# Kernel optimization log

Measured on AMD Instinct MI355X. Metric: run time of the kernel, lower is better.

## Reference

```python
import jax, jax.numpy as jnp
import numpy as np
import math

HID = 128      # hidden_dim == d_inner (expand=1)
NSTATE = 8     # d_state
K = 4          # scan directions
RANK = math.ceil(HID / 16)  # dt_rank = 8
B, H, W = 4, 64, 64


def _ln(x, g, b, eps=1e-5):
    m = jnp.mean(x, -1, keepdims=True)
    v = jnp.mean((x - m) ** 2, -1, keepdims=True)
    return (x - m) * jax.lax.rsqrt(v + eps) * g + b


def _ss2d(x, in_w, conv_w, conv_b, xproj_w, dt_w, dt_b, A_logs, Ds, ln_g, ln_b, out_w):
    # x: [B,H,W,C] -> VMamba SS2D with d_inner=C, 4-direction selective scan
    Bn, Hh, Ww, C = x.shape
    D, L = C, Hh * Ww
    N = A_logs.shape[-1]
    R = dt_w.shape[-1]
    xz = x @ in_w.T                      # [B,H,W,2D]
    xc, z = jnp.split(xz, 2, axis=-1)
    xc = xc.transpose(0, 3, 1, 2)        # [B,D,H,W]
    xc = jax.lax.conv_general_dilated(xc, conv_w, (1, 1), 'SAME', feature_group_count=D)
    xc = jax.nn.silu(xc + conv_b[None, :, None, None])
    x_hw = xc.reshape(Bn, D, L)
    x_wh = xc.transpose(0, 1, 3, 2).reshape(Bn, D, L)
    xs = jnp.stack([x_hw, x_wh, x_hw[..., ::-1], x_wh[..., ::-1]], 1)  # [B,K,D,L]
    x_dbl = jnp.einsum('bkdl,kcd->bkcl', xs, xproj_w)
    dts, Bs, Cs = x_dbl[:, :, :R], x_dbl[:, :, R:R + N], x_dbl[:, :, R + N:]
    dt = jax.nn.softplus(jnp.einsum('bkrl,kdr->bkdl', dts, dt_w) + dt_b[None, :, :, None])
    A = -jnp.exp(A_logs.reshape(K, D, N))  # [K,D,N]

    def step(h, inp):
        x_t, dt_t, B_t, C_t = inp          # [B,K,D],[B,K,D],[B,K,N],[B,K,N]
        h = h * jnp.exp(dt_t[..., None] * A) + dt_t[..., None] * B_t[:, :, None, :] * x_t[..., None]
        return h, jnp.einsum('bkdn,bkn->bkd', h, C_t)

    h0 = jnp.zeros((Bn, K, D, N), x.dtype)
    _, ys = jax.lax.scan(step, h0, (xs.transpose(3, 0, 1, 2), dt.transpose(3, 0, 1, 2),
                                    Bs.transpose(3, 0, 1, 2), Cs.transpose(3, 0, 1, 2)))
    out_y = ys.transpose(1, 2, 3, 0) + Ds.reshape(K, D)[None, :, :, None] * xs  # [B,K,D,L]
    wh_y = out_y[:, 3, :, ::-1].reshape(Bn, D, Ww, Hh).transpose(0, 1, 3, 2).reshape(Bn, D, L)
    invwh_y = out_y[:, 1].reshape(Bn, D, Ww, Hh).transpose(0, 1, 3, 2).reshape(Bn, D, L)
    y = out_y[:, 0] + out_y[:, 2, :, ::-1] + wh_y + invwh_y
    y = _ln(y.transpose(0, 2, 1).reshape(Bn, Hh, Ww, D), ln_g, ln_b)
    return (y * jax.nn.silu(z)) @ out_w.T


def _enhance(x, g, b, w, bias):
    return jax.nn.gelu(_ln(x, g, b) @ w.T + bias, approximate=False)


def setup_inputs() -> dict:
    key = jax.random.key(0)
    ks = jax.random.split(key, 12)
    f = lambda k, s, sc=0.02: jax.random.normal(k, s, jnp.float32) * sc
    return dict(
        sar_feat=jax.random.normal(ks[0], (B, H, W, HID), jnp.float32),
        opt_feat=jax.random.normal(ks[1], (B, H, W, HID), jnp.float32),
        ss_in_w=f(ks[2], (2, 2 * HID, HID)),
        ss_conv_w=f(ks[3], (2, HID, 1, 3, 3), 0.1),
        ss_conv_b=f(ks[4], (2, HID)),
        ss_xproj_w=f(ks[5], (2, K, RANK + 2 * NSTATE, HID)),
        ss_dt_w=f(ks[6], (2, K, HID, RANK), 0.1),
        ss_dt_b=f(ks[7], (2, K, HID), 0.1),
        ss_Alogs=jnp.tile(jnp.log(jnp.arange(1, NSTATE + 1, dtype=jnp.float32)), (2, K * HID, 1)),
        ss_Ds=jnp.ones((2, K * HID), jnp.float32),
        ss_ln_g=jnp.ones((2, HID), jnp.float32),
        ss_ln_b=jnp.zeros((2, HID), jnp.float32),
        ss_out_w=f(ks[8], (2, HID, HID)),
        enh_ln_g=jnp.ones((2, HID), jnp.float32),
        enh_ln_b=jnp.zeros((2, HID), jnp.float32),
        enh_w=f(ks[9], (2, HID, HID)),
        enh_b=jnp.zeros((2, HID), jnp.float32),
    )


def reference(sar_feat, opt_feat, ss_in_w, ss_conv_w, ss_conv_b, ss_xproj_w, ss_dt_w,
              ss_dt_b, ss_Alogs, ss_Ds, ss_ln_g, ss_ln_b, ss_out_w,
              enh_ln_g, enh_ln_b, enh_w, enh_b):
    # cat([opt,sar],-1)[...,:C] == opt ; cat([sar,opt],-1)[...,:C] == sar (faithful identity slice)
    # index 0 = cross_ss2d_s2o (input opt), index 1 = cross_ss2d_o2s (input sar)
    xin = jnp.stack([opt_feat, sar_feat])
    guided = jax.vmap(_ss2d)(xin, ss_in_w, ss_conv_w, ss_conv_b, ss_xproj_w, ss_dt_w,
                             ss_dt_b, ss_Alogs, ss_Ds, ss_ln_g, ss_ln_b, ss_out_w)
    # enhance params: index 0 = enhance_sar (on sar_guided=guided[1]), index 1 = enhance_opt (on opt_guided=guided[0])
    enh_in = jnp.stack([guided[1], guided[0]])
    enhanced = jax.vmap(_enhance)(enh_in, enh_ln_g, enh_ln_b, enh_w, enh_b)
    return (sar_feat + enhanced[0], opt_feat + enhanced[1])
```

## Files before the change

### kernel.cpp

```cpp
#include <hip/hip_runtime.h>
#include <hip/hip_bf16.h>
#include <math.h>

#define DEV __device__ __forceinline__

static constexpr int LL = 4096;
static constexpr int DD = 128;
static constexpr int SEG = 128;
static constexpr float LOG2E = 1.4426950408889634f;
static constexpr float LN2 = 0.6931471805599453f;

DEV float silu_(float x) { return x / (1.f + __expf(-x)); }
DEV float erf_(float x) {
  const float ax = fabsf(x);
  const float t = 1.f / fmaf(0.3275911f, ax, 1.f);
  float p = fmaf(1.061405429f, t, -1.453152027f);
  p = fmaf(p, t, 1.421413741f);
  p = fmaf(p, t, -0.284496736f);
  p = fmaf(p, t, 0.254829592f);
  p = p * t;
  const float r = 1.f - p * __expf(-ax * ax);
  return x < 0.f ? -r : r;
}
DEV float gelu_(float x) { return 0.5f * x * (1.f + erf_(x * 0.7071067811865475f)); }
DEV float sp_(float x) {
  const float t = __builtin_amdgcn_exp2f(-fabsf(x) * LOG2E);
  return fmaxf(x, 0.f) + LN2 * __builtin_amdgcn_logf(1.f + t);
}

template <int CTRL>
DEV float dpp_add_(float x) {
  int y = __builtin_amdgcn_update_dpp(0, __float_as_int(x), CTRL, 0xF, 0xF, true);
  return x + __int_as_float(y);
}

DEV void seg_base_step(int k, int s, int& base, int& step) {
  if (k == 0)      { base = s * 64;        step = 1;   }
  else if (k == 1) { base = s;             step = 64;  }
  else if (k == 2) { base = 4095 - s * 64; step = -1;  }
  else             { base = 4095 - s;      step = -64; }
}

__global__ __launch_bounds__(256) void k_inproj(
    const float* __restrict__ sar, const float* __restrict__ opt,
    const float* __restrict__ in_w, float* __restrict__ xz) {
  const int lt = blockIdx.x, ct = blockIdx.y, mb = blockIdx.z;
  const int m = mb >> 2;
  const float* __restrict__ x = (m == 0 ? opt : sar) + (size_t)(mb & 3) * (LL * DD);
  const float* __restrict__ W = in_w + (size_t)m * 256 * DD;
  __shared__ float sA[64][68];
  __shared__ float sW[64][68];
  const int tid = threadIdx.x;
  const int tc = tid & 15, tl = tid >> 4;
  float acc[4][4] = {};
  for (int db = 0; db < 2; ++db) {
    __syncthreads();
    for (int idx = tid; idx < 64 * 16; idx += 256) {
      const int r = idx >> 4, d4 = (idx & 15) << 2;
      *(float4*)&sA[r][d4] = *(const float4*)&x[(size_t)(lt * 64 + r) * DD + db * 64 + d4];
      *(float4*)&sW[r][d4] = *(const float4*)&W[(size_t)(ct * 64 + r) * DD + db * 64 + d4];
    }
    __syncthreads();
#pragma unroll 4
    for (int d = 0; d < 64; d += 4) {
      float4 a[4], w[4];
#pragma unroll
      for (int q = 0; q < 4; ++q) a[q] = *(const float4*)&sA[tl * 4 + q][d];
#pragma unroll
      for (int j = 0; j < 4; ++j) w[j] = *(const float4*)&sW[tc + 16 * j][d];
#pragma unroll
      for (int j = 0; j < 4; ++j)
#pragma unroll
        for (int q = 0; q < 4; ++q)
          acc[j][q] += a[q].x * w[j].x + a[q].y * w[j].y + a[q].z * w[j].z + a[q].w * w[j].w;
    }
  }
  float* __restrict__ dst = xz + ((size_t)mb * 256 + ct * 64) * LL + lt * 64;
#pragma unroll
  for (int j = 0; j < 4; ++j) {
    float4 v = make_float4(acc[j][0], acc[j][1], acc[j][2], acc[j][3]);
    *(float4*)&dst[(size_t)(tc + 16 * j) * LL + tl * 4] = v;
  }
}

__global__ __launch_bounds__(256) void k_conv(
    const float* __restrict__ xz, const float* __restrict__ conv_w,
    const float* __restrict__ conv_b, float* __restrict__ xc) {
  const int ht = blockIdx.x, dg = blockIdx.y, mb = blockIdx.z;
  const int m = mb >> 2;
  __shared__ float sIn[8][18][66];
  __shared__ float sOut[1024][8];
  const float* __restrict__ src = xz + ((size_t)mb * 256 + dg * 8) * LL;
  const int tid = threadIdx.x;
  for (int idx = tid; idx < 8 * 18 * 66; idx += 256) {
    const int dd = idx / (18 * 66);
    const int rem = idx - dd * (18 * 66);
    const int hh = rem / 66, ww = rem - hh * 66;
    const int h = ht * 16 + hh - 1, w = ww - 1;
    float v = 0.f;
    if (h >= 0 && h < 64 && w >= 0 && w < 64) v = src[(size_t)dd * LL + h * 64 + w];
    sIn[dd][hh][ww] = v;
  }
  __syncthreads();
  const int dd = tid & 7, wv = tid >> 3;
  const int dch = dg * 8 + dd;
  float wk[9];
#pragma unroll
  for (int t = 0; t < 9; ++t) wk[t] = conv_w[((size_t)m * DD + dch) * 9 + t];
  const float bias = conv_b[m * DD + dch];
  for (int hh = 0; hh < 16; ++hh) {
#pragma unroll
    for (int wh = 0; wh < 2; ++wh) {
      const int w = wv + wh * 32;
      float s = bias;
#pragma unroll
      for (int kh = 0; kh < 3; ++kh)
#pragma unroll
        for (int kw = 0; kw < 3; ++kw)
          s = fmaf(sIn[dd][hh + kh][w + kw], wk[kh * 3 + kw], s);
      sOut[hh * 64 + w][dd] = silu_(s);
    }
  }
  __syncthreads();
  float* __restrict__ dst = xc + (size_t)mb * LL * DD + dg * 8;
#pragma unroll
  for (int r = 0; r < 4; ++r) {
    const int pos = tid + r * 256;
    const int l = ht * 1024 + pos;
    *(float4*)&dst[(size_t)l * DD + 0] = *(const float4*)&sOut[pos][0];
    *(float4*)&dst[(size_t)l * DD + 4] = *(const float4*)&sOut[pos][4];
  }
}

__global__ __launch_bounds__(256) void k_xproj(
    const float* __restrict__ xc, const float* __restrict__ xproj_w,
    float* __restrict__ xdbl) {
  const int lt = blockIdx.x, k = blockIdx.y, mb = blockIdx.z;
  const int m = mb >> 2, mbk = mb * 4 + k;
  __shared__ float sX[64][132];
  __shared__ float sW[24][132];
  const int tid = threadIdx.x;
  const float* __restrict__ src = xc + (size_t)mb * LL * DD;
  int base, step;
  seg_base_step(k, lt, base, step);
  for (int idx = tid; idx < 64 * 32; idx += 256) {
    const int l = idx >> 5, d4 = (idx & 31) << 2;
    *(float4*)&sX[l][d4] = *(const float4*)&src[(size_t)(base + l * step) * DD + d4];
  }
  const float* __restrict__ Wsrc = xproj_w + ((size_t)m * 4 + k) * 24 * DD;
  for (int idx = tid; idx < 24 * 32; idx += 256) {
    const int r = idx >> 5, d4 = (idx & 31) << 2;
    *(float4*)&sW[r][d4] = *(const float4*)&Wsrc[(size_t)r * DD + d4];
  }
  __syncthreads();
  const int l = tid >> 2, cg = tid & 3;
  float acc[6] = {};
#pragma unroll 8
  for (int d = 0; d < 128; d += 4) {
    const float4 xv = *(const float4*)&sX[l][d];
#pragma unroll
    for (int j = 0; j < 6; ++j) {
      const float4 wv = *(const float4*)&sW[cg * 6 + j][d];
      acc[j] += xv.x * wv.x + xv.y * wv.y + xv.z * wv.z + xv.w * wv.w;
    }
  }
  float* __restrict__ dst = xdbl + ((size_t)mbk * LL + lt * 64 + l) * 24 + cg * 6;
#pragma unroll
  for (int j = 0; j < 6; ++j) dst[j] = acc[j];
}

DEV void load_aln2(const float* __restrict__ Alogs, int m, int k, int d,
                   float* __restrict__ aln2, bool& fastp) {
  const float4 a0 = *(const float4*)&Alogs[((size_t)m * 512 + k * DD + d) * 8];
  const float4 a1 = *(const float4*)&Alogs[((size_t)m * 512 + k * DD + d) * 8 + 4];
  aln2[0] = -__expf(a0.x) * LOG2E; aln2[1] = -__expf(a0.y) * LOG2E;
  aln2[2] = -__expf(a0.z) * LOG2E; aln2[3] = -__expf(a0.w) * LOG2E;
  aln2[4] = -__expf(a1.x) * LOG2E; aln2[5] = -__expf(a1.y) * LOG2E;
  aln2[6] = -__expf(a1.z) * LOG2E; aln2[7] = -__expf(a1.w) * LOG2E;
  fastp = true;
#pragma unroll
  for (int n = 1; n < 8; ++n)
    fastp = fastp && (fabsf(aln2[n] - (float)(n + 1) * aln2[0]) <=
                      1e-4f * fabsf(aln2[n]) + 1e-12f);
}

DEV void load_w8(const float* __restrict__ dt_w, int mbk, int d,
                 float* __restrict__ wreg) {
  const float4 w0 = *(const float4*)&dt_w[((size_t)mbk * DD + d) * 8];
  const float4 w1 = *(const float4*)&dt_w[((size_t)mbk * DD + d) * 8 + 4];
  wreg[0] = w0.x; wreg[1] = w0.y; wreg[2] = w0.z; wreg[3] = w0.w;
  wreg[4] = w1.x; wreg[5] = w1.y; wreg[6] = w1.z; wreg[7] = w1.w;
}

template <bool FAST>
DEV void qpow_(float dt, const float* __restrict__ aln2, float* __restrict__ q) {
  if constexpr (FAST) {
    q[0] = __builtin_amdgcn_exp2f(dt * aln2[0]);
    q[1] = q[0] * q[0]; q[2] = q[1] * q[0]; q[3] = q[1] * q[1];
    q[4] = q[3] * q[0]; q[5] = q[3] * q[1]; q[6] = q[3] * q[2]; q[7] = q[3] * q[3];
  } else {
#pragma unroll
    for (int n = 0; n < 8; ++n) q[n] = __builtin_amdgcn_exp2f(dt * aln2[n]);
  }
}

DEV float dt_of_(const float* __restrict__ t24,
                 const float* __restrict__ w, float bw) {
  const float4 t0 = *(const float4*)&t24[0];
  const float4 t1 = *(const float4*)&t24[4];
  float s = bw;
  s = fmaf(t0.x, w[0], s); s = fmaf(t0.y, w[1], s);
  s = fmaf(t0.z, w[2], s); s = fmaf(t0.w, w[3], s);
  s = fmaf(t1.x, w[4], s); s = fmaf(t1.y, w[5], s);
  s = fmaf(t1.z, w[6], s); s = fmaf(t1.w, w[7], s);
  return sp_(s);
}

template <bool FAST>
DEV void hstep_(const float* __restrict__ t24, float dt, float x,
                const float* __restrict__ aln2, float* __restrict__ h) {
  const float u = dt * x;
  float q[8];
  qpow_<FAST>(dt, aln2, q);
  const float4 b0 = *(const float4*)&t24[8];
  const float4 b1 = *(const float4*)&t24[12];
  h[0] = fmaf(h[0], q[0], u * b0.x);
  h[1] = fmaf(h[1], q[1], u * b0.y);
  h[2] = fmaf(h[2], q[2], u * b0.z);
  h[3] = fmaf(h[3], q[3], u * b0.w);
  h[4] = fmaf(h[4], q[4], u * b1.x);
  h[5] = fmaf(h[5], q[5], u * b1.y);
  h[6] = fmaf(h[6], q[6], u * b1.z);
  h[7] = fmaf(h[7], q[7], u * b1.w);
}

template <bool FAST>
DEV float ystep_(const float* __restrict__ t24, float dt, float x,
                 const float* __restrict__ aln2, float dsv,
                 float* __restrict__ h) {
  const float u = dt * x;
  float q[8];
  qpow_<FAST>(dt, aln2, q);
  const float4 b0 = *(const float4*)&t24[8];
  const float4 b1 = *(const float4*)&t24[12];
  const float4 c0 = *(const float4*)&t24[16];
  const float4 c1 = *(const float4*)&t24[20];
  float y = dsv * x;
  h[0] = fmaf(h[0], q[0], u * b0.x); y = fmaf(h[0], c0.x, y);
  h[1] = fmaf(h[1], q[1], u * b0.y); y = fmaf(h[1], c0.y, y);
  h[2] = fmaf(h[2], q[2], u * b0.z); y = fmaf(h[2], c0.z, y);
  h[3] = fmaf(h[3], q[3], u * b0.w); y = fmaf(h[3], c0.w, y);
  h[4] = fmaf(h[4], q[4], u * b1.x); y = fmaf(h[4], c1.x, y);
  h[5] = fmaf(h[5], q[5], u * b1.y); y = fmaf(h[5], c1.y, y);
  h[6] = fmaf(h[6], q[6], u * b1.z); y = fmaf(h[6], c1.z, y);
  h[7] = fmaf(h[7], q[7], u * b1.w); y = fmaf(h[7], c1.w, y);
  return y;
}

template <bool FAST>
DEV void loop1d_(const float* __restrict__ tA, const float* __restrict__ tB,
                 const float* __restrict__ sx, int d,
                 const float* __restrict__ aln2A, const float* __restrict__ aln2B,
                 const float* __restrict__ wA, const float* __restrict__ wB,
                 float bwA, float bwB, float* __restrict__ hA,
                 float* __restrict__ hB, float& dtsA, float& dtsB) {
#pragma unroll 8
  for (int j = 0; j < 32; ++j) {
    const float xA = sx[j * 128 + d];
    const float xB = sx[(31 - j) * 128 + d];
    const float dtA = dt_of_(tA + j * 24, wA, bwA);
    const float dtB = dt_of_(tB + j * 24, wB, bwB);
    dtsA += dtA; dtsB += dtB;
    hstep_<FAST>(tA + j * 24, dtA, xA, aln2A, hA);
    hstep_<FAST>(tB + j * 24, dtB, xB, aln2B, hB);
  }
}

__global__ __launch_bounds__(128) void k_scan1(
    const float* __restrict__ xc, const float* __restrict__ xdbl,
    const float* __restrict__ dt_w, const float* __restrict__ dt_b,
    const float* __restrict__ Alogs, float* __restrict__ hend,
    float* __restrict__ Pseg) {
  const int s = blockIdx.x, p = blockIdx.y, mb = blockIdx.z;
  const int m = mb >> 2;
  const int kA = p, kB = p + 2;
  const int sA = s, sB = 127 - s;
  const int mbkA = mb * 4 + kA, mbkB = mb * 4 + kB;
  const int d = threadIdx.x;
  __shared__ float sx[32 * 128];

  const float* __restrict__ tA = xdbl + ((size_t)mbkA * LL + sA * 32) * 24;
  const float* __restrict__ tB = xdbl + ((size_t)mbkB * LL + sB * 32) * 24;

  const int base0 = (p == 0) ? s * 32 : ((s & 1) * 32) * 64 + (s >> 1);
  const int stepPos = (p == 0) ? 1 : 64;
  const float* __restrict__ xsrc = xc + (size_t)mb * LL * DD;
#pragma unroll
  for (int t = 0; t < 8; ++t) {
    const int idx = d + t * 128;
    const int r = idx >> 5, c4 = (idx & 31) << 2;
    ((float4*)sx)[idx] = *(const float4*)&xsrc[(size_t)(base0 + r * stepPos) * DD + c4];
  }

  float aln2A[8], aln2B[8]; bool fA, fB;
  load_aln2(Alogs, m, kA, d, aln2A, fA);
  load_aln2(Alogs, m, kB, d, aln2B, fB);
  float wA[8], wB[8];
  load_w8(dt_w, mbkA, d, wA);
  load_w8(dt_w, mbkB, d, wB);
  const float bwA = dt_b[(size_t)mbkA * DD + d];
  const float bwB = dt_b[(size_t)mbkB * DD + d];
  __syncthreads();

  float hA[8] = {0, 0, 0, 0, 0, 0, 0, 0};
  float hB[8] = {0, 0, 0, 0, 0, 0, 0, 0};
  float dtsA = 0.f, dtsB = 0.f;
  if (fA && fB)
    loop1d_<true>(tA, tB, sx, d, aln2A, aln2B, wA, wB, bwA, bwB, hA, hB, dtsA, dtsB);
  else
    loop1d_<false>(tA, tB, sx, d, aln2A, aln2B, wA, wB, bwA, bwB, hA, hB, dtsA, dtsB);

  {
    float* __restrict__ he = hend + (((size_t)mbkA * SEG + sA) << 10) + d * 8;
    float* __restrict__ pe = Pseg + (((size_t)mbkA * SEG + sA) << 10) + d * 8;
    *(float4*)&he[0] = make_float4(hA[0], hA[1], hA[2], hA[3]);
    *(float4*)&he[4] = make_float4(hA[4], hA[5], hA[6], hA[7]);
    *(float4*)&pe[0] = make_float4(
        __builtin_amdgcn_exp2f(aln2A[0] * dtsA), __builtin_amdgcn_exp2f(aln2A[1] * dtsA),
        __builtin_amdgcn_exp2f(aln2A[2] * dtsA), __builtin_amdgcn_exp2f(aln2A[3] * dtsA));
    *(float4*)&pe[4] = make_float4(
        __builtin_amdgcn_exp2f(aln2A[4] * dtsA), __builtin_amdgcn_exp2f(aln2A[5] * dtsA),
        __builtin_amdgcn_exp2f(aln2A[6] * dtsA), __builtin_amdgcn_exp2f(aln2A[7] * dtsA));
  }
  {
    float* __restrict__ he = hend + (((size_t)mbkB * SEG + sB) << 10) + d * 8;
    float* __restrict__ pe = Pseg + (((size_t)mbkB * SEG + sB) << 10) + d * 8;
    *(float4*)&he[0] = make_float4(hB[0], hB[1], hB[2], hB[3]);
    *(float4*)&he[4] = make_float4(hB[4], hB[5], hB[6], hB[7]);
    *(float4*)&pe[0] = make_float4(
        __builtin_amdgcn_exp2f(aln2B[0] * dtsB), __builtin_amdgcn_exp2f(aln2B[1] * dtsB),
        __builtin_amdgcn_exp2f(aln2B[2] * dtsB), __builtin_amdgcn_exp2f(aln2B[3] * dtsB));
    *(float4*)&pe[4] = make_float4(
        __builtin_amdgcn_exp2f(aln2B[4] * dtsB), __builtin_amdgcn_exp2f(aln2B[5] * dtsB),
        __builtin_amdgcn_exp2f(aln2B[6] * dtsB), __builtin_amdgcn_exp2f(aln2B[7] * dtsB));
  }
}

__global__ __launch_bounds__(256) void k_scan2(
    const float* __restrict__ hend, const float* __restrict__ Pseg,
    float* __restrict__ hin) {
  const int gid = blockIdx.x * 256 + threadIdx.x;
  const int mbk = gid >> 10, dn = gid & 1023;
  const float* __restrict__ P = Pseg + ((size_t)mbk * SEG << 10) + dn;
  const float* __restrict__ E = hend + ((size_t)mbk * SEG << 10) + dn;
  float* __restrict__ O = hin + ((size_t)mbk * SEG << 10) + dn;
  float h = 0.f;
  for (int c0 = 0; c0 < SEG; c0 += 16) {
    float pv[16], ev[16];
#pragma unroll
    for (int t = 0; t < 16; ++t) {
      pv[t] = P[(size_t)(c0 + t) << 10];
      ev[t] = E[(size_t)(c0 + t) << 10];
    }
#pragma unroll
    for (int t = 0; t < 16; ++t) {
      O[(size_t)(c0 + t) << 10] = h;
      h = fmaf(pv[t], h, ev[t]);
    }
  }
}

template <bool FAST>
DEV void chainA_(const float* __restrict__ t24, const float* __restrict__ sx, int d,
                 const float* __restrict__ aln2, const float* __restrict__ w,
                 float bw, float dsv, float* __restrict__ h,
                 float* __restrict__ va) {
#pragma unroll
  for (int j = 0; j < 32; ++j) {
    const float x = sx[j * 128 + d];
    const float dt = dt_of_(t24 + j * 24, w, bw);
    va[j] = ystep_<FAST>(t24 + j * 24, dt, x, aln2, dsv, h);
  }
}

template <bool FAST>
DEV void chainB_(const float* __restrict__ t24, const float* __restrict__ sx, int d,
                 const float* __restrict__ aln2, const float* __restrict__ w,
                 float bw, float dsv, float* __restrict__ h,
                 const float* __restrict__ va, float* __restrict__ yd,
                 ptrdiff_t sstep) {
#pragma unroll
  for (int j = 0; j < 32; ++j) {
    const int phys = 31 - j;
    const float x = sx[phys * 128 + d];
    const float dt = dt_of_(t24 + j * 24, w, bw);
    const float v = ystep_<FAST>(t24 + j * 24, dt, x, aln2, dsv, h);
    yd[(ptrdiff_t)phys * sstep] = v + va[phys];
  }
}

__global__ __launch_bounds__(128) void k_scan3(
    const float* __restrict__ xc, const float* __restrict__ xdbl,
    const float* __restrict__ dt_w, const float* __restrict__ dt_b,
    const float* __restrict__ Alogs, const float* __restrict__ Ds,
    const float* __restrict__ hin, float* __restrict__ yrow,
    float* __restrict__ ycol) {
  const int s = blockIdx.x, p = blockIdx.y, mb = blockIdx.z;
  const int m = mb >> 2;
  const int kA = p, kB = p + 2;
  const int sA = s, sB = 127 - s;
  const int mbkA = mb * 4 + kA, mbkB = mb * 4 + kB;
  const int d = threadIdx.x;
  __shared__ float sx[32 * 128];

  const float* __restrict__ tA = xdbl + ((size_t)mbkA * LL + sA * 32) * 24;
  const float* __restrict__ tB = xdbl + ((size_t)mbkB * LL + sB * 32) * 24;

  const int base0 = (p == 0) ? s * 32 : ((s & 1) * 32) * 64 + (s >> 1);
  const int stepPos = (p == 0) ? 1 : 64;
  const float* __restrict__ xsrc = xc + (size_t)mb * LL * DD;
#pragma unroll
  for (int t = 0; t < 8; ++t) {
    const int idx = d + t * 128;
    const int r = idx >> 5, c4 = (idx & 31) << 2;
    ((float4*)sx)[idx] = *(const float4*)&xsrc[(size_t)(base0 + r * stepPos) * DD + c4];
  }

  float aln2A[8], aln2B[8]; bool fA, fB;
  load_aln2(Alogs, m, kA, d, aln2A, fA);
  load_aln2(Alogs, m, kB, d, aln2B, fB);
  float wA[8], wB[8];
  load_w8(dt_w, mbkA, d, wA);
  load_w8(dt_w, mbkB, d, wB);
  const float bwA = dt_b[(size_t)mbkA * DD + d];
  const float bwB = dt_b[(size_t)mbkB * DD + d];
  const float dsvA = Ds[(size_t)m * 512 + kA * DD + d];
  const float dsvB = Ds[(size_t)m * 512 + kB * DD + d];

  float hA[8], hB[8];
  {
    const float* hp = hin + (((size_t)mbkA * SEG + sA) << 10) + d * 8;
    const float4 h0 = *(const float4*)&hp[0];
    const float4 h1 = *(const float4*)&hp[4];
    hA[0] = h0.x; hA[1] = h0.y; hA[2] = h0.z; hA[3] = h0.w;
    hA[4] = h1.x; hA[5] = h1.y; hA[6] = h1.z; hA[7] = h1.w;
  }
  {
    const float* hp = hin + (((size_t)mbkB * SEG + sB) << 10) + d * 8;
    const float4 h0 = *(const float4*)&hp[0];
    const float4 h1 = *(const float4*)&hp[4];
    hB[0] = h0.x; hB[1] = h0.y; hB[2] = h0.z; hB[3] = h0.w;
    hB[4] = h1.x; hB[5] = h1.y; hB[6] = h1.z; hB[7] = h1.w;
  }

  const size_t off0 = (size_t)mb * LL * DD + (size_t)base0 * DD + d;
  float* __restrict__ yd = (p == 0 ? yrow : ycol) + off0;
  const ptrdiff_t sstep = (ptrdiff_t)stepPos * DD;
  __syncthreads();

  float va[32];
  if (fA) chainA_<true>(tA, sx, d, aln2A, wA, bwA, dsvA, hA, va);
  else    chainA_<false>(tA, sx, d, aln2A, wA, bwA, dsvA, hA, va);
  if (fB) chainB_<true>(tB, sx, d, aln2B, wB, bwB, dsvB, hB, va, yd, sstep);
  else    chainB_<false>(tB, sx, d, aln2B, wB, bwB, dsvB, hB, va, yd, sstep);
}

__global__ __launch_bounds__(256) void k_outproj(
    const float* __restrict__ yrow, const float* __restrict__ ycol,
    const float* __restrict__ xz, const float* __restrict__ ln_g,
    const float* __restrict__ ln_b, const float* __restrict__ out_w,
    float* __restrict__ guided) {
  const int lt = blockIdx.x, mb = blockIdx.y;
  const int m = mb >> 2;
  __shared__ float sv[32][132];
  __shared__ float sW[64][68];
  __shared__ float smr[32][2];
  __shared__ float sg[128], sb[128];
  const int tid = threadIdx.x;
  const size_t yoff = ((size_t)mb * LL + lt * 32) * DD;
  const float4* p0 = (const float4*)(yrow + yoff);
  const float4* p1 = (const float4*)(ycol + yoff);
  float4 ya[4], yb[4];
#pragma unroll
  for (int t = 0; t < 4; ++t) { ya[t] = p0[tid + t * 256]; yb[t] = p1[tid + t * 256]; }
  const int zc = tid >> 1, zh = tid & 1;
  const float4* zsrc = (const float4*)(xz + ((size_t)mb * 256 + 128 + zc) * LL + lt * 32 + zh * 16);
  float4 zv[4];
#pragma unroll
  for (int t = 0; t < 4; ++t) zv[t] = zsrc[t];
  const float* __restrict__ Wp = out_w + (size_t)m * DD * DD;
  float4 wpre[4];
#pragma unroll
  for (int t = 0; t < 4; ++t) {
    const int idx = tid + t * 256;
    wpre[t] = *(const float4*)&Wp[(size_t)(idx >> 4) * DD + ((idx & 15) << 2)];
  }
  if (tid < 128) { sg[tid] = ln_g[m * DD + tid]; sb[tid] = ln_b[m * DD + tid]; }
#pragma unroll
  for (int t = 0; t < 4; ++t) {
    const int idx = tid + t * 256;
    float4 v;
    v.x = ya[t].x + yb[t].x; v.y = ya[t].y + yb[t].y;
    v.z = ya[t].z + yb[t].z; v.w = ya[t].w + yb[t].w;
    *(float4*)&sv[idx >> 5][(idx & 31) << 2] = v;
  }
  __syncthreads();
  {
    const int l = tid >> 3, q = tid & 7;
    float s = 0.f, s2 = 0.f;
#pragma unroll
    for (int d0 = 0; d0 < 16; d0 += 4) {
      const float4 v = *(const float4*)&sv[l][q * 16 + d0];
      s += v.x + v.y + v.z + v.w;
      s2 += v.x * v.x + v.y * v.y + v.z * v.z + v.w * v.w;
    }
    s = dpp_add_<0xB1>(s); s = dpp_add_<0x4E>(s); s = dpp_add_<0x141>(s);
    s2 = dpp_add_<0xB1>(s2); s2 = dpp_add_<0x4E>(s2); s2 = dpp_add_<0x141>(s2);
    if (q == 0) {
      const float mean = s * (1.f / 128.f);
      smr[l][0] = mean;
      smr[l][1] = rsqrtf(fmaf(s2, 1.f / 128.f, -mean * mean) + 1e-5f);
    }
  }
  __syncthreads();
  {
    const float g = sg[zc], bb = sb[zc];
    const float* zf = (const float*)zv;
#pragma unroll
    for (int i2 = 0; i2 < 16; ++i2) {
      const int l = zh * 16 + i2;
      const float v = fmaf((sv[l][zc] - smr[l][0]) * smr[l][1], g, bb);
      sv[l][zc] = v * silu_(zf[i2]);
    }
  }
  const int tc = tid & 15, tl = tid >> 4;
  float* __restrict__ dst = guided + ((size_t)mb * LL + lt * 32) * DD;
  float accA[4][2] = {}, accB[4][2] = {};
#pragma unroll
  for (int jb = 0; jb < 2; ++jb) {
#pragma unroll
    for (int db = 0; db < 2; ++db) {
      __syncthreads();
#pragma unroll
      for (int t = 0; t < 4; ++t) {
        const int idx = tid + t * 256;
        *(float4*)&sW[idx >> 4][(idx & 15) << 2] = wpre[t];
      }
      const int ph = jb * 2 + db + 1;
      if (ph < 4) {
        const int jb2 = ph >> 1, db2 = ph & 1;
#pragma unroll
        for (int t = 0; t < 4; ++t) {
          const int idx = tid + t * 256;
          wpre[t] = *(const float4*)&Wp[(size_t)(jb2 * 64 + (idx >> 4)) * DD + db2 * 64 + ((idx & 15) << 2)];
        }
      }
      __syncthreads();
      float (*acc)[2] = (jb == 0) ? accA : accB;
#pragma unroll 4
      for (int d0 = 0; d0 < 64; d0 += 4) {
        float4 av[2], wv[4];
#pragma unroll
        for (int q = 0; q < 2; ++q) av[q] = *(const float4*)&sv[tl * 2 + q][db * 64 + d0];
#pragma unroll
        for (int j = 0; j < 4; ++j) wv[j] = *(const float4*)&sW[tc + 16 * j][d0];
#pragma unroll
        for (int j = 0; j < 4; ++j)
#pragma unroll
          for (int q = 0; q < 2; ++q)
            acc[j][q] += av[q].x * wv[j].x + av[q].y * wv[j].y + av[q].z * wv[j].z + av[q].w * wv[j].w;
      }
    }
  }
  __syncthreads();
#pragma unroll
  for (int jb = 0; jb < 2; ++jb)
#pragma unroll
    for (int j = 0; j < 4; ++j)
#pragma unroll
      for (int q = 0; q < 2; ++q)
        sv[tl * 2 + q][jb * 64 + tc + 16 * j] = (jb == 0) ? accA[j][q] : accB[j][q];
  __syncthreads();
#pragma unroll
  for (int t = 0; t < 4; ++t) {
    const int idx = tid + t * 256;
    const int row = idx >> 5, c4 = (idx & 31) << 2;
    *(float4*)&dst[(size_t)row * DD + c4] = *(const float4*)&sv[row][c4];
  }
}

__global__ __launch_bounds__(256) void k_enhance(
    const float* __restrict__ guided, const float* __restrict__ eg,
    const float* __restrict__ ebv, const float* __restrict__ ew,
    const float* __restrict__ ebias, const float* __restrict__ sar,
    const float* __restrict__ opt, float* __restrict__ outp) {
  const int lt = blockIdx.x, ib = blockIdx.y;
  const int i = ib >> 2, b = ib & 3;
  __shared__ float sv[32][132];
  __shared__ float sW[64][68];
  __shared__ float smr[32][2];
  __shared__ float sg[128], sb2[128], sbias[128];
  const int tid = threadIdx.x;
  const float4* gsrc =
      (const float4*)(guided + (((size_t)(1 - i) * 4 + b) * LL + lt * 32) * DD);
  float4 gv[4];
#pragma unroll
  for (int t = 0; t < 4; ++t) gv[t] = gsrc[tid + t * 256];
  const float* __restrict__ resid = (i == 0 ? sar : opt) + ((size_t)b * LL + lt * 32) * DD;
  float4 rv4[4];
#pragma unroll
  for (int t = 0; t < 4; ++t) {
    const int idx = tid + t * 256;
    rv4[t] = *(const float4*)&resid[(size_t)(idx >> 5) * DD + ((idx & 31) << 2)];
  }
  const float* __restrict__ Wp = ew + (size_t)i * DD * DD;
  float4 wpre[4];
#pragma unroll
  for (int t = 0; t < 4; ++t) {
    const int idx = tid + t * 256;
    wpre[t] = *(const float4*)&Wp[(size_t)(idx >> 4) * DD + ((idx & 15) << 2)];
  }
  if (tid < 128) {
    sg[tid] = eg[i * DD + tid];
    sb2[tid] = ebv[i * DD + tid];
    sbias[tid] = ebias[i * DD + tid];
  }
#pragma unroll
  for (int t = 0; t < 4; ++t) {
    const int idx = tid + t * 256;
    *(float4*)&sv[idx >> 5][(idx & 31) << 2] = gv[t];
  }
  __syncthreads();
  {
    const int l = tid >> 3, q = tid & 7;
    float s = 0.f, s2 = 0.f;
#pragma unroll
    for (int d0 = 0; d0 < 16; d0 += 4) {
      const float4 v = *(const float4*)&sv[l][q * 16 + d0];
      s += v.x + v.y + v.z + v.w;
      s2 += v.x * v.x + v.y * v.y + v.z * v.z + v.w * v.w;
    }
    s = dpp_add_<0xB1>(s); s = dpp_add_<0x4E>(s); s = dpp_add_<0x141>(s);
    s2 = dpp_add_<0xB1>(s2); s2 = dpp_add_<0x4E>(s2); s2 = dpp_add_<0x141>(s2);
    if (q == 0) {
      const float mean = s * (1.f / 128.f);
      smr[l][0] = mean;
      smr[l][1] = rsqrtf(fmaf(s2, 1.f / 128.f, -mean * mean) + 1e-5f);
    }
  }
  __syncthreads();
  {
    const int c = tid >> 1, half = tid & 1;
    const float g = sg[c], bb = sb2[c];
#pragma unroll
    for (int i2 = 0; i2 < 16; ++i2) {
      const int l = half * 16 + i2;
      sv[l][c] = fmaf((sv[l][c] - smr[l][0]) * smr[l][1], g, bb);
    }
  }
  const int tc = tid & 15, tl = tid >> 4;
  float* __restrict__ dst = outp + (size_t)i * (4 * LL * DD) + ((size_t)b * LL + lt * 32) * DD;
  float accA[4][2] = {}, accB[4][2] = {};
#pragma unroll
  for (int jb = 0; jb < 2; ++jb) {
#pragma unroll
    for (int db = 0; db < 2; ++db) {
      __syncthreads();
#pragma unroll
      for (int t = 0; t < 4; ++t) {
        const int idx = tid + t * 256;
        *(float4*)&sW[idx >> 4][(idx & 15) << 2] = wpre[t];
      }
      const int ph = jb * 2 + db + 1;
      if (ph < 4) {
        const int jb2 = ph >> 1, db2 = ph & 1;
#pragma unroll
        for (int t = 0; t < 4; ++t) {
          const int idx = tid + t * 256;
          wpre[t] = *(const float4*)&Wp[(size_t)(jb2 * 64 + (idx >> 4)) * DD + db2 * 64 + ((idx & 15) << 2)];
        }
      }
      __syncthreads();
      float (*acc)[2] = (jb == 0) ? accA : accB;
#pragma unroll 4
      for (int d0 = 0; d0 < 64; d0 += 4) {
        float4 av[2], wv[4];
#pragma unroll
        for (int q = 0; q < 2; ++q) av[q] = *(const float4*)&sv[tl * 2 + q][db * 64 + d0];
#pragma unroll
        for (int j = 0; j < 4; ++j) wv[j] = *(const float4*)&sW[tc + 16 * j][d0];
#pragma unroll
        for (int j = 0; j < 4; ++j)
#pragma unroll
          for (int q = 0; q < 2; ++q)
            acc[j][q] += av[q].x * wv[j].x + av[q].y * wv[j].y + av[q].z * wv[j].z + av[q].w * wv[j].w;
      }
    }
  }
  __syncthreads();
#pragma unroll
  for (int jb = 0; jb < 2; ++jb)
#pragma unroll
    for (int j = 0; j < 4; ++j)
#pragma unroll
      for (int q = 0; q < 2; ++q)
        sv[tl * 2 + q][jb * 64 + tc + 16 * j] = (jb == 0) ? accA[j][q] : accB[j][q];
  __syncthreads();
#pragma unroll
  for (int t = 0; t < 4; ++t) {
    const int idx = tid + t * 256;
    const int row = idx >> 5, c4 = (idx & 31) << 2;
    const float4 a = *(const float4*)&sv[row][c4];
    const float4 bia = *(const float4*)&sbias[c4];
    float4 o;
    o.x = rv4[t].x + gelu_(a.x + bia.x);
    o.y = rv4[t].y + gelu_(a.y + bia.y);
    o.z = rv4[t].z + gelu_(a.z + bia.z);
    o.w = rv4[t].w + gelu_(a.w + bia.w);
    *(float4*)&dst[(size_t)row * DD + c4] = o;
  }
}

extern "C" void kernel_launch(void* const* d_in, const int* in_sizes, int n_in,
                              void* d_out, int out_size, void* d_ws, size_t ws_size,
                              hipStream_t stream) {
  (void)in_sizes; (void)n_in; (void)out_size; (void)ws_size;
  const float* sar    = (const float*)d_in[0];
  const float* opt    = (const float*)d_in[1];
  const float* in_w   = (const float*)d_in[2];
  const float* conv_w = (const float*)d_in[3];
  const float* conv_b = (const float*)d_in[4];
  const float* xproj_w= (const float*)d_in[5];
  const float* dt_w   = (const float*)d_in[6];
  const float* dt_b   = (const float*)d_in[7];
  const float* Alogs  = (const float*)d_in[8];
  const float* Ds     = (const float*)d_in[9];
  const float* ln_g   = (const float*)d_in[10];
  const float* ln_b   = (const float*)d_in[11];
  const float* out_w  = (const float*)d_in[12];
  const float* eg     = (const float*)d_in[13];
  const float* eb     = (const float*)d_in[14];
  const float* ew     = (const float*)d_in[15];
  const float* ebias  = (const float*)d_in[16];

  float* ws     = (float*)d_ws;
  float* xz     = ws;
  float* xc     = xz + 8388608;
  float* xdbl   = xc + 4194304;
  float* yrowb  = xdbl + 3145728;
  float* ycolb  = yrowb + 4194304;
  float* guided = ycolb + 4194304;
  float* hend   = guided + 4194304;
  float* Pseg   = hend + 4194304;
  float* hin    = Pseg + 4194304;
  float* outf   = (float*)d_out;

  k_inproj <<<dim3(64, 4, 8), 256, 0, stream>>>(sar, opt, in_w, xz);
  k_conv   <<<dim3(4, 16, 8), 256, 0, stream>>>(xz, conv_w, conv_b, xc);
  k_xproj  <<<dim3(64, 4, 8), 256, 0, stream>>>(xc, xproj_w, xdbl);
  k_scan1  <<<dim3(128, 2, 8), 128, 0, stream>>>(xc, xdbl, dt_w, dt_b, Alogs, hend, Pseg);
  k_scan2  <<<dim3(128), 256, 0, stream>>>(hend, Pseg, hin);
  k_scan3  <<<dim3(128, 2, 8), 128, 0, stream>>>(xc, xdbl, dt_w, dt_b, Alogs, Ds, hin,
                                                 yrowb, ycolb);
  k_outproj<<<dim3(128, 8), 256, 0, stream>>>(yrowb, ycolb, xz, ln_g, ln_b, out_w, guided);
  k_enhance<<<dim3(128, 8), 256, 0, stream>>>(guided, eg, eb, ew, ebias, sar, opt, outf);
}
```

Measured before the change: 266.0 us.

## Precompute dt in fp16 once and fuse paired-direction xproj

```diff
diff --git a/kernel.cpp b/kernel.cpp
--- a/kernel.cpp
+++ b/kernel.cpp
@@ -1,5 +1,6 @@
 #include <hip/hip_runtime.h>
 #include <hip/hip_bf16.h>
+#include <hip/hip_fp16.h>
 #include <math.h>
 
 #define DEV __device__ __forceinline__
@@ -135,38 +136,46 @@
 __global__ __launch_bounds__(256) void k_xproj(
     const float* __restrict__ xc, const float* __restrict__ xproj_w,
     float* __restrict__ xdbl) {
-  const int lt = blockIdx.x, k = blockIdx.y, mb = blockIdx.z;
-  const int m = mb >> 2, mbk = mb * 4 + k;
+  const int lt = blockIdx.x, p = blockIdx.y, mb = blockIdx.z;
+  const int m = mb >> 2;
+  const int mbkA = mb * 4 + p, mbkB = mb * 4 + p + 2;
   __shared__ float sX[64][132];
-  __shared__ float sW[24][132];
+  __shared__ float sWA[24][132];
+  __shared__ float sWB[24][132];
   const int tid = threadIdx.x;
   const float* __restrict__ src = xc + (size_t)mb * LL * DD;
   int base, step;
-  seg_base_step(k, lt, base, step);
+  seg_base_step(p, lt, base, step);
   for (int idx = tid; idx < 64 * 32; idx += 256) {
     const int l = idx >> 5, d4 = (idx & 31) << 2;
     *(float4*)&sX[l][d4] = *(const float4*)&src[(size_t)(base + l * step) * DD + d4];
   }
-  const float* __restrict__ Wsrc = xproj_w + ((size_t)m * 4 + k) * 24 * DD;
+  const float* __restrict__ WsA = xproj_w + ((size_t)m * 4 + p) * 24 * DD;
+  const float* __restrict__ WsB = xproj_w + ((size_t)m * 4 + p + 2) * 24 * DD;
   for (int idx = tid; idx < 24 * 32; idx += 256) {
     const int r = idx >> 5, d4 = (idx & 31) << 2;
-    *(float4*)&sW[r][d4] = *(const float4*)&Wsrc[(size_t)r * DD + d4];
+    *(float4*)&sWA[r][d4] = *(const float4*)&WsA[(size_t)r * DD + d4];
+    *(float4*)&sWB[r][d4] = *(const float4*)&WsB[(size_t)r * DD + d4];
   }
   __syncthreads();
   const int l = tid >> 2, cg = tid & 3;
-  float acc[6] = {};
+  float acc[6] = {}, acc2[6] = {};
 #pragma unroll 8
   for (int d = 0; d < 128; d += 4) {
     const float4 xv = *(const float4*)&sX[l][d];
 #pragma unroll
     for (int j = 0; j < 6; ++j) {
-      const float4 wv = *(const float4*)&sW[cg * 6 + j][d];
-      acc[j] += xv.x * wv.x + xv.y * wv.y + xv.z * wv.z + xv.w * wv.w;
-    }
-  }
-  float* __restrict__ dst = xdbl + ((size_t)mbk * LL + lt * 64 + l) * 24 + cg * 6;
-#pragma unroll
-  for (int j = 0; j < 6; ++j) dst[j] = acc[j];
+      const float4 wa = *(const float4*)&sWA[cg * 6 + j][d];
+      const float4 wb = *(const float4*)&sWB[cg * 6 + j][d];
+      acc[j] += xv.x * wa.x + xv.y * wa.y + xv.z * wa.z + xv.w * wa.w;
+      acc2[j] += xv.x * wb.x + xv.y * wb.y + xv.z * wb.z + xv.w * wb.w;
+    }
+  }
+  const int rowA = lt * 64 + l;
+  float* __restrict__ dstA = xdbl + ((size_t)mbkA * LL + rowA) * 24 + cg * 6;
+  float* __restrict__ dstB = xdbl + ((size_t)mbkB * LL + (4095 - rowA)) * 24 + cg * 6;
+#pragma unroll
+  for (int j = 0; j < 6; ++j) { dstA[j] = acc[j]; dstB[j] = acc2[j]; }
 }
 
 DEV void load_aln2(const float* __restrict__ Alogs, int m, int k, int d,
@@ -257,19 +266,37 @@
   return y;
 }
 
+__global__ __launch_bounds__(256) void k_dtpre(
+    const float* __restrict__ xdbl, const float* __restrict__ dt_w,
+    const float* __restrict__ dt_b, __half* __restrict__ dtp) {
+  const int bx = blockIdx.x, mbk = blockIdx.y;
+  const int tid = threadIdx.x;
+  const int d = tid & 127, ph = tid >> 7;
+  float wreg[8];
+  load_w8(dt_w, mbk, d, wreg);
+  const float bw = dt_b[(size_t)mbk * DD + d];
+  const int pos0 = bx * 64 + ph * 32;
+  const float* __restrict__ t = xdbl + ((size_t)mbk * LL + pos0) * 24;
+  __half* __restrict__ out = dtp + ((size_t)mbk * LL + pos0) * DD + d;
+#pragma unroll 8
+  for (int j = 0; j < 32; ++j)
+    out[j * DD] = __float2half(dt_of_(t + j * 24, wreg, bw));
+}
+
+
 template <bool FAST>
 DEV void loop1d_(const float* __restrict__ tA, const float* __restrict__ tB,
+                 const __half* __restrict__ dtpA, const __half* __restrict__ dtpB,
                  const float* __restrict__ sx, int d,
                  const float* __restrict__ aln2A, const float* __restrict__ aln2B,
-                 const float* __restrict__ wA, const float* __restrict__ wB,
-                 float bwA, float bwB, float* __restrict__ hA,
-                 float* __restrict__ hB, float& dtsA, float& dtsB) {
+                 float* __restrict__ hA, float* __restrict__ hB,
+                 float& dtsA, float& dtsB) {
 #pragma unroll 8
   for (int j = 0; j < 32; ++j) {
     const float xA = sx[j * 128 + d];
     const float xB = sx[(31 - j) * 128 + d];
-    const float dtA = dt_of_(tA + j * 24, wA, bwA);
-    const float dtB = dt_of_(tB + j * 24, wB, bwB);
+    const float dtA = __half2float(dtpA[j * DD]);
+    const float dtB = __half2float(dtpB[j * DD]);
     dtsA += dtA; dtsB += dtB;
     hstep_<FAST>(tA + j * 24, dtA, xA, aln2A, hA);
     hstep_<FAST>(tB + j * 24, dtB, xB, aln2B, hB);
@@ -278,9 +305,8 @@
 
 __global__ __launch_bounds__(128) void k_scan1(
     const float* __restrict__ xc, const float* __restrict__ xdbl,
-    const float* __restrict__ dt_w, const float* __restrict__ dt_b,
-    const float* __restrict__ Alogs, float* __restrict__ hend,
-    float* __restrict__ Pseg) {
+    const __half* __restrict__ dtp, const float* __restrict__ Alogs,
+    float* __restrict__ hend, float* __restrict__ Pseg) {
   const int s = blockIdx.x, p = blockIdx.y, mb = blockIdx.z;
   const int m = mb >> 2;
   const int kA = p, kB = p + 2;
@@ -291,6 +317,8 @@
 
   const float* __restrict__ tA = xdbl + ((size_t)mbkA * LL + sA * 32) * 24;
   const float* __restrict__ tB = xdbl + ((size_t)mbkB * LL + sB * 32) * 24;
+  const __half* __restrict__ dtpA = dtp + ((size_t)mbkA * LL + sA * 32) * DD + d;
+  const __half* __restrict__ dtpB = dtp + ((size_t)mbkB * LL + sB * 32) * DD + d;
 
   const int base0 = (p == 0) ? s * 32 : ((s & 1) * 32) * 64 + (s >> 1);
   const int stepPos = (p == 0) ? 1 : 64;
@@ -305,20 +333,15 @@
   float aln2A[8], aln2B[8]; bool fA, fB;
   load_aln2(Alogs, m, kA, d, aln2A, fA);
   load_aln2(Alogs, m, kB, d, aln2B, fB);
-  float wA[8], wB[8];
-  load_w8(dt_w, mbkA, d, wA);
-  load_w8(dt_w, mbkB, d, wB);
-  const float bwA = dt_b[(size_t)mbkA * DD + d];
-  const float bwB = dt_b[(size_t)mbkB * DD + d];
   __syncthreads();
 
   float hA[8] = {0, 0, 0, 0, 0, 0, 0, 0};
   float hB[8] = {0, 0, 0, 0, 0, 0, 0, 0};
   float dtsA = 0.f, dtsB = 0.f;
   if (fA && fB)
-    loop1d_<true>(tA, tB, sx, d, aln2A, aln2B, wA, wB, bwA, bwB, hA, hB, dtsA, dtsB);
+    loop1d_<true>(tA, tB, dtpA, dtpB, sx, d, aln2A, aln2B, hA, hB, dtsA, dtsB);
   else
-    loop1d_<false>(tA, tB, sx, d, aln2A, aln2B, wA, wB, bwA, bwB, hA, hB, dtsA, dtsB);
+    loop1d_<false>(tA, tB, dtpA, dtpB, sx, d, aln2A, aln2B, hA, hB, dtsA, dtsB);
 
   {
     float* __restrict__ he = hend + (((size_t)mbkA * SEG + sA) << 10) + d * 8;
@@ -371,29 +394,29 @@
 }
 
 template <bool FAST>
-DEV void chainA_(const float* __restrict__ t24, const float* __restrict__ sx, int d,
-                 const float* __restrict__ aln2, const float* __restrict__ w,
-                 float bw, float dsv, float* __restrict__ h,
-                 float* __restrict__ va) {
+DEV void chainA_(const float* __restrict__ t24, const __half* __restrict__ dtpc,
+                 const float* __restrict__ sx, int d,
+                 const float* __restrict__ aln2, float dsv,
+                 float* __restrict__ h, float* __restrict__ va) {
 #pragma unroll
   for (int j = 0; j < 32; ++j) {
     const float x = sx[j * 128 + d];
-    const float dt = dt_of_(t24 + j * 24, w, bw);
+    const float dt = __half2float(dtpc[j * DD]);
     va[j] = ystep_<FAST>(t24 + j * 24, dt, x, aln2, dsv, h);
   }
 }
 
 template <bool FAST>
-DEV void chainB_(const float* __restrict__ t24, const float* __restrict__ sx, int d,
-                 const float* __restrict__ aln2, const float* __restrict__ w,
-                 float bw, float dsv, float* __restrict__ h,
-                 const float* __restrict__ va, float* __restrict__ yd,
-                 ptrdiff_t sstep) {
+DEV void chainB_(const float* __restrict__ t24, const __half* __restrict__ dtpc,
+                 const float* __restrict__ sx, int d,
+                 const float* __restrict__ aln2, float dsv,
+                 float* __restrict__ h, const float* __restrict__ va,
+                 float* __restrict__ yd, ptrdiff_t sstep) {
 #pragma unroll
   for (int j = 0; j < 32; ++j) {
     const int phys = 31 - j;
     const float x = sx[phys * 128 + d];
-    const float dt = dt_of_(t24 + j * 24, w, bw);
+    const float dt = __half2float(dtpc[j * DD]);
     const float v = ystep_<FAST>(t24 + j * 24, dt, x, aln2, dsv, h);
     yd[(ptrdiff_t)phys * sstep] = v + va[phys];
   }
@@ -401,10 +424,9 @@
 
 __global__ __launch_bounds__(128) void k_scan3(
     const float* __restrict__ xc, const float* __restrict__ xdbl,
-    const float* __restrict__ dt_w, const float* __restrict__ dt_b,
-    const float* __restrict__ Alogs, const float* __restrict__ Ds,
-    const float* __restrict__ hin, float* __restrict__ yrow,
-    float* __restrict__ ycol) {
+    const __half* __restrict__ dtp, const float* __restrict__ Alogs,
+    const float* __restrict__ Ds, const float* __restrict__ hin,
+    float* __restrict__ yrow, float* __restrict__ ycol) {
   const int s = blockIdx.x, p = blockIdx.y, mb = blockIdx.z;
   const int m = mb >> 2;
   const int kA = p, kB = p + 2;
@@ -415,6 +437,8 @@
 
   const float* __restrict__ tA = xdbl + ((size_t)mbkA * LL + sA * 32) * 24;
   const float* __restrict__ tB = xdbl + ((size_t)mbkB * LL + sB * 32) * 24;
+  const __half* __restrict__ dtpA = dtp + ((size_t)mbkA * LL + sA * 32) * DD + d;
+  const __half* __restrict__ dtpB = dtp + ((size_t)mbkB * LL + sB * 32) * DD + d;
 
   const int base0 = (p == 0) ? s * 32 : ((s & 1) * 32) * 64 + (s >> 1);
   const int stepPos = (p == 0) ? 1 : 64;
@@ -429,11 +453,6 @@
   float aln2A[8], aln2B[8]; bool fA, fB;
   load_aln2(Alogs, m, kA, d, aln2A, fA);
   load_aln2(Alogs, m, kB, d, aln2B, fB);
-  float wA[8], wB[8];
-  load_w8(dt_w, mbkA, d, wA);
-  load_w8(dt_w, mbkB, d, wB);
-  const float bwA = dt_b[(size_t)mbkA * DD + d];
-  const float bwB = dt_b[(size_t)mbkB * DD + d];
   const float dsvA = Ds[(size_t)m * 512 + kA * DD + d];
   const float dsvB = Ds[(size_t)m * 512 + kB * DD + d];
 
@@ -459,10 +478,10 @@
   __syncthreads();
 
   float va[32];
-  if (fA) chainA_<true>(tA, sx, d, aln2A, wA, bwA, dsvA, hA, va);
-  else    chainA_<false>(tA, sx, d, aln2A, wA, bwA, dsvA, hA, va);
-  if (fB) chainB_<true>(tB, sx, d, aln2B, wB, bwB, dsvB, hB, va, yd, sstep);
-  else    chainB_<false>(tB, sx, d, aln2B, wB, bwB, dsvB, hB, va, yd, sstep);
+  if (fA) chainA_<true>(tA, dtpA, sx, d, aln2A, dsvA, hA, va);
+  else    chainA_<false>(tA, dtpA, sx, d, aln2A, dsvA, hA, va);
+  if (fB) chainB_<true>(tB, dtpB, sx, d, aln2B, dsvB, hB, va, yd, sstep);
+  else    chainB_<false>(tB, dtpB, sx, d, aln2B, dsvB, hB, va, yd, sstep);
 }
 
 __global__ __launch_bounds__(256) void k_outproj(
@@ -749,18 +768,20 @@
   float* xdbl   = xc + 4194304;
   float* yrowb  = xdbl + 3145728;
   float* ycolb  = yrowb + 4194304;
-  float* guided = ycolb + 4194304;
-  float* hend   = guided + 4194304;
+  float* hend   = ycolb + 4194304;
   float* Pseg   = hend + 4194304;
   float* hin    = Pseg + 4194304;
+  __half* dtpre = (__half*)(hin + 4194304);
+  float* guided = hin;
   float* outf   = (float*)d_out;
 
   k_inproj <<<dim3(64, 4, 8), 256, 0, stream>>>(sar, opt, in_w, xz);
   k_conv   <<<dim3(4, 16, 8), 256, 0, stream>>>(xz, conv_w, conv_b, xc);
-  k_xproj  <<<dim3(64, 4, 8), 256, 0, stream>>>(xc, xproj_w, xdbl);
-  k_scan1  <<<dim3(128, 2, 8), 128, 0, stream>>>(xc, xdbl, dt_w, dt_b, Alogs, hend, Pseg);
+  k_xproj  <<<dim3(64, 2, 8), 256, 0, stream>>>(xc, xproj_w, xdbl);
+  k_dtpre  <<<dim3(64, 32), 256, 0, stream>>>(xdbl, dt_w, dt_b, dtpre);
+  k_scan1  <<<dim3(128, 2, 8), 128, 0, stream>>>(xc, xdbl, dtpre, Alogs, hend, Pseg);
   k_scan2  <<<dim3(128), 256, 0, stream>>>(hend, Pseg, hin);
-  k_scan3  <<<dim3(128, 2, 8), 128, 0, stream>>>(xc, xdbl, dt_w, dt_b, Alogs, Ds, hin,
+  k_scan3  <<<dim3(128, 2, 8), 128, 0, stream>>>(xc, xdbl, dtpre, Alogs, Ds, hin,
                                                  yrowb, ycolb);
   k_outproj<<<dim3(128, 8), 256, 0, stream>>>(yrowb, ycolb, xz, ln_g, ln_b, out_w, guided);
   k_enhance<<<dim3(128, 8), 256, 0, stream>>>(guided, eg, eb, ew, ebias, sar, opt, outf);
```

After: 279.4 us. +5.0%, slower.
